# Optimization experiments

Measured on AMD Instinct MI355X. Metric: run time of the kernel, lower is better.

## Reference

```python
import jax, jax.numpy as jnp
import numpy as np

N = 8192
IN_DIM = 256
OUT_DIM = 128
ALPHA = 0.2  # LeakyReLU negative slope
MASK_VAL = -9e15


def setup_inputs() -> dict:
    key = jax.random.key(0)
    k1, k2, k3, k4 = jax.random.split(key, 4)
    adjacency = jax.random.randint(k1, (N, N), 0, 2, dtype=jnp.int32)
    X = jax.random.normal(k2, (N, IN_DIM), dtype=jnp.float32)
    # kaiming-normal-ish scale
    W = jax.random.normal(k3, (IN_DIM, OUT_DIM), dtype=jnp.float32) * np.sqrt(2.0 / IN_DIM)
    a = jax.random.normal(k4, (2 * OUT_DIM, 1), dtype=jnp.float32) * np.sqrt(2.0 / (2 * OUT_DIM))
    return {"adjacency": adjacency, "X": X, "W": W, "a": a}


def reference(adjacency, X, W, a):
    Wh = X @ W  # [N, D]
    # e[i,j] = lrelu([Wh_i ; Wh_j] @ a) = lrelu(Wh@a1 + (Wh@a2)^T)
    a1 = a[:OUT_DIM, 0]   # [D]
    a2 = a[OUT_DIM:, 0]   # [D]
    e = (Wh @ a1)[:, None] + (Wh @ a2)[None, :]  # [N, N]
    e = jax.nn.leaky_relu(e, negative_slope=ALPHA)
    scores = jnp.where(adjacency > 0, e, jnp.asarray(MASK_VAL, e.dtype))
    attention = jax.nn.softmax(scores, axis=1)  # dropout p=0 -> identity
    h_prime = attention @ Wh  # [N, D]
    return jax.nn.elu(h_prime)
```

## Files before the change

kernel.cpp:

```cpp
#include <hip/hip_runtime.h>
#include <hip/hip_bf16.h>

#define NN 8192
#define KDIM 256
#define DDIM 128

typedef __attribute__((ext_vector_type(8))) short short8;
typedef __attribute__((ext_vector_type(4))) float floatx4;
typedef __attribute__((ext_vector_type(4))) int intx4;

__device__ __forceinline__ unsigned short f2bf(float x) {
    unsigned int u = __float_as_uint(x);
    return (unsigned short)((u + 0x8000u) >> 16);
}

__global__ void k_trip(float* out, float v) {
    if (threadIdx.x == 0 && blockIdx.x == 0) out[0] = v;
}

__global__ void kA_swizzleW(const float* __restrict__ W, unsigned short* __restrict__ WB) {
    int gid = blockIdx.x * blockDim.x + threadIdx.x;
    int kt = gid >> 9, nt = (gid >> 6) & 7, lane = gid & 63;
    int quad = lane >> 4, c = lane & 15;
    short8 pack;
#pragma unroll
    for (int t = 0; t < 8; ++t)
        pack[t] = (short)f2bf(W[(kt * 32 + quad * 8 + t) * DDIM + nt * 16 + c]);
    *(short8*)(WB + ((size_t)(kt * 8 + nt) * 64 + lane) * 8) = pack;
}

__global__ __launch_bounds__(256) void kB_wh(
        const float* __restrict__ X,
        const unsigned short* __restrict__ WB,
        const float* __restrict__ a,
        unsigned short* __restrict__ WhB,
        float* __restrict__ f, float* __restrict__ g) {
    __shared__ unsigned short tile[64 * 128];
    int tid = threadIdx.x;
    int wave = tid >> 6, lane = tid & 63;
    int quad = lane >> 4, c = lane & 15;
    int rowbase = blockIdx.x * 64 + wave * 16;

    floatx4 acc[8];
#pragma unroll
    for (int nt = 0; nt < 8; ++nt) acc[nt] = (floatx4)(0.0f);

    const short8* WB8 = (const short8*)WB;
#pragma unroll
    for (int ks = 0; ks < 8; ++ks) {
        const float* xp = X + (size_t)(rowbase + c) * KDIM + ks * 32 + quad * 8;
        floatx4 x0 = *(const floatx4*)xp;
        floatx4 x1 = *(const floatx4*)(xp + 4);
        short8 afrag;
#pragma unroll
        for (int t = 0; t < 4; ++t) { afrag[t] = (short)f2bf(x0[t]); afrag[4 + t] = (short)f2bf(x1[t]); }
#pragma unroll
        for (int nt = 0; nt < 8; ++nt) {
            short8 b = WB8[(ks * 8 + nt) * 64 + lane];
            acc[nt] = __builtin_amdgcn_mfma_f32_16x16x32_bf16(afrag, b, acc[nt], 0, 0, 0);
        }
    }

    float fp[4] = {0.f, 0.f, 0.f, 0.f}, gp[4] = {0.f, 0.f, 0.f, 0.f};
#pragma unroll
    for (int nt = 0; nt < 8; ++nt) {
        float a1 = a[nt * 16 + c];
        float a2 = a[DDIM + nt * 16 + c];
#pragma unroll
        for (int r = 0; r < 4; ++r) {
            fp[r] += acc[nt][r] * a1;
            gp[r] += acc[nt][r] * a2;
        }
    }
#pragma unroll
    for (int m = 1; m < 16; m <<= 1) {
#pragma unroll
        for (int r = 0; r < 4; ++r) {
            fp[r] += __shfl_xor(fp[r], m);
            gp[r] += __shfl_xor(gp[r], m);
        }
    }
    if (c == 0) {
#pragma unroll
        for (int r = 0; r < 4; ++r) {
            f[rowbase + quad * 4 + r] = fp[r];
            g[rowbase + quad * 4 + r] = gp[r];
        }
    }

#pragma unroll
    for (int nt = 0; nt < 8; ++nt)
#pragma unroll
        for (int r = 0; r < 4; ++r)
            tile[(wave * 16 + quad * 4 + r) * 128 + nt * 16 + c] = f2bf(acc[nt][r]);
    __syncthreads();

    int kt2 = wave >> 1;
#pragma unroll
    for (int ntj = 0; ntj < 4; ++ntj) {
        int nt = (wave & 1) * 4 + ntj;
        short8 pack;
#pragma unroll
        for (int t = 0; t < 8; ++t)
            pack[t] = (short)tile[(kt2 * 32 + quad * 8 + t) * 128 + nt * 16 + c];
        *(short8*)(WhB + ((size_t)((blockIdx.x * 2 + kt2) * 8 + nt) * 64 + lane) * 8) = pack;
    }
}

__global__ __launch_bounds__(256, 4) void kC_attn2(
        const int* __restrict__ adj,
        const unsigned short* __restrict__ WhB,
        const float* __restrict__ f, const float* __restrict__ g,
        float* __restrict__ pacc, float* __restrict__ pl) {
    __shared__ float smem[8192];
    int tid = threadIdx.x;
    int wave = tid >> 6, lane = tid & 63;
    int quad = lane >> 4, c = lane & 15;
    int bq   = blockIdx.x >> 9;
    int brow = blockIdx.x & 511;
    int rowbase = brow * 16;

    {
        const floatx4* g4 = (const floatx4*)g;
        for (int i = tid; i < 1024; i += 256)
            ((floatx4*)smem)[i] = g4[bq * 1024 + i];
    }
    __syncthreads();

    float f0 = f[rowbase + c];

    floatx4 acc[8];
#pragma unroll
    for (int nt = 0; nt < 8; ++nt) acc[nt] = (floatx4)(0.0f);
    float l0 = 0.0f;

    const intx4* arow = (const intx4*)(adj + (size_t)(rowbase + c) * NN);
    const short8* WhB8 = (const short8*)WhB;
    int jbase = bq * 128;

    intx4 A0a = __builtin_nontemporal_load(&arow[(jbase + 0 * 4 + wave) * 8 + quad * 2]);
    intx4 A0b = __builtin_nontemporal_load(&arow[(jbase + 0 * 4 + wave) * 8 + quad * 2 + 1]);
    intx4 A1a = __builtin_nontemporal_load(&arow[(jbase + 1 * 4 + wave) * 8 + quad * 2]);
    intx4 A1b = __builtin_nontemporal_load(&arow[(jbase + 1 * 4 + wave) * 8 + quad * 2 + 1]);

    short8 bfrA[8], bfrB[8];
#pragma unroll
    for (int nt = 0; nt < 8; ++nt)
        bfrA[nt] = WhB8[((size_t)(jbase + wave) * 8 + nt) * 64 + lane];

#define KC_STEP(ITC, BCUR, BNEXT) do {                                          \
        int J32n_ = jbase + (((ITC) + 1) & 31) * 4 + wave;                      \
        _Pragma("unroll")                                                       \
        for (int nt = 0; nt < 8; ++nt)                                          \
            BNEXT[nt] = WhB8[((size_t)J32n_ * 8 + nt) * 64 + lane];             \
        int j4n_ = jbase + (((ITC) + 2) & 31) * 4 + wave;                       \
        intx4 A2a_ = __builtin_nontemporal_load(&arow[j4n_ * 8 + quad * 2]);    \
        intx4 A2b_ = __builtin_nontemporal_load(&arow[j4n_ * 8 + quad * 2 + 1]);\
        int gb_ = ((ITC) * 4 + wave) * 32 + quad * 8;                           \
        floatx4 g0_ = *(const floatx4*)&smem[gb_];                              \
        floatx4 g1_ = *(const floatx4*)&smem[gb_ + 4];                          \
        short8 afr_;                                                            \
        _Pragma("unroll")                                                       \
        for (int u = 0; u < 4; ++u) {                                           \
            float x_, E_;                                                       \
            x_ = f0 + g0_[u]; x_ = fmaxf(x_, 0.2f * x_);                        \
            E_ = (A0a[u] > 0) ? __expf(x_) : 0.0f; l0 += E_;                    \
            afr_[u] = (short)f2bf(E_);                                          \
            x_ = f0 + g1_[u]; x_ = fmaxf(x_, 0.2f * x_);                        \
            E_ = (A0b[u] > 0) ? __expf(x_) : 0.0f; l0 += E_;                    \
            afr_[4 + u] = (short)f2bf(E_);                                      \
        }                                                                       \
        _Pragma("unroll")                                                       \
        for (int nt = 0; nt < 8; ++nt)                                          \
            acc[nt] = __builtin_amdgcn_mfma_f32_16x16x32_bf16(afr_, BCUR[nt],   \
                                                              acc[nt], 0, 0, 0);\
        A0a = A1a; A0b = A1b; A1a = A2a_; A1b = A2b_;                           \
    } while (0)

    for (int it = 0; it < 32; it += 2) {
        KC_STEP(it, bfrA, bfrB);
        KC_STEP(it + 1, bfrB, bfrA);
    }
#undef KC_STEP

    __syncthreads();
    smem[7000 + wave * 64 + lane] = l0;
    __syncthreads();
    if (tid < 16) {
        float s = 0.0f;
#pragma unroll
        for (int w = 0; w < 4; ++w)
#pragma unroll
            for (int q = 0; q < 4; ++q)
                s += smem[7000 + w * 64 + q * 16 + tid];
        pl[bq * NN + rowbase + tid] = s;
    }

    if (wave >= 2) {
        float* b = &smem[(wave - 2) * 2304 + lane * 36];
#pragma unroll
        for (int nt = 0; nt < 8; ++nt) *(floatx4*)&b[nt * 4] = acc[nt];
    }
    __syncthreads();
    if (wave < 2) {
        float* b = &smem[wave * 2304 + lane * 36];
#pragma unroll
        for (int nt = 0; nt < 8; ++nt) acc[nt] += *(const floatx4*)&b[nt * 4];
    }
    __syncthreads();
    if (wave == 1) {
        float* b = &smem[lane * 36];
#pragma unroll
        for (int nt = 0; nt < 8; ++nt) *(floatx4*)&b[nt * 4] = acc[nt];
    }
    __syncthreads();

    if (wave == 0) {
        float* b = &smem[lane * 36];
#pragma unroll
        for (int nt = 0; nt < 8; ++nt) acc[nt] += *(const floatx4*)&b[nt * 4];
        float* pb = pacc + (size_t)bq * NN * DDIM;
#pragma unroll
        for (int nt = 0; nt < 8; ++nt)
#pragma unroll
            for (int r = 0; r < 4; ++r)
                pb[(size_t)(rowbase + quad * 4 + r) * DDIM + nt * 16 + c] = acc[nt][r];
    }
}

__global__ __launch_bounds__(256) void kD_merge2(
        const float* __restrict__ pacc, const float* __restrict__ pl,
        float* __restrict__ out) {
    int i = blockIdx.x * 256 + threadIdx.x;
    const floatx4* p4 = (const floatx4*)pacc;
    floatx4 a = p4[i];
    floatx4 b = p4[i + NN * DDIM / 4];
    int row = i >> 5;
    float s = pl[row] + pl[NN + row];
    float inv = (s > 0.0f) ? 1.0f / s : 0.0f;
    floatx4 h;
#pragma unroll
    for (int r = 0; r < 4; ++r) {
        float v = (a[r] + b[r]) * inv;
        h[r] = (v > 0.0f) ? v : expm1f(v);
    }
    ((floatx4*)out)[i] = h;
}

extern "C" void kernel_launch(void* const* d_in, const int* in_sizes, int n_in,
                              void* d_out, int out_size, void* d_ws, size_t ws_size,
                              hipStream_t stream) {
    float* out = (float*)d_out;

    const void *p_adj = nullptr, *p_X = nullptr, *p_W = nullptr, *p_a = nullptr;
    for (int i = 0; i < n_in; ++i) {
        switch (in_sizes[i]) {
            case NN * NN:     p_adj = d_in[i]; break;
            case NN * KDIM:   p_X   = d_in[i]; break;
            case KDIM * DDIM: p_W   = d_in[i]; break;
            case 2 * DDIM:    p_a   = d_in[i]; break;
            default: break;
        }
    }
    if (!p_adj || !p_X || !p_W || !p_a) {
        k_trip<<<dim3(1), dim3(64), 0, stream>>>(out, 99999.0f);
        return;
    }

    size_t off_WB   = 0;
    size_t off_WhB  = off_WB + 65536;
    size_t off_f    = off_WhB + (size_t)NN * DDIM * 2;
    size_t off_g    = off_f + NN * 4;
    size_t off_pacc = off_g + NN * 4;
    size_t off_pl   = off_pacc + (size_t)2 * NN * DDIM * 4;
    size_t needed   = off_pl + (size_t)2 * NN * 4;
    if (ws_size < needed) {
        k_trip<<<dim3(1), dim3(64), 0, stream>>>(out, 12345.0f);
        return;
    }
    char* ws = (char*)d_ws;
    unsigned short* WB   = (unsigned short*)(ws + off_WB);
    unsigned short* WhB  = (unsigned short*)(ws + off_WhB);
    float*          f    = (float*)(ws + off_f);
    float*          g    = (float*)(ws + off_g);
    float*          pacc = (float*)(ws + off_pacc);
    float*          pl   = (float*)(ws + off_pl);

    const int*   adj = (const int*)p_adj;
    const float* X   = (const float*)p_X;
    const float* W   = (const float*)p_W;
    const float* a   = (const float*)p_a;

    kA_swizzleW<<<dim3(16), dim3(256), 0, stream>>>(W, WB);
    kB_wh<<<dim3(128), dim3(256), 0, stream>>>(X, WB, a, WhB, f, g);
    kC_attn2<<<dim3(1024), dim3(256), 0, stream>>>(adj, WhB, f, g, pacc, pl);
    kD_merge2<<<dim3(NN * DDIM / 4 / 256), dim3(256), 0, stream>>>(pacc, pl, out);
}
```

Baseline: 435.7 us.

## Switch attention kernel to 32x32 MFMA with per-wave D split and 4-way column split

The attention kernel now uses 32x32x16 bf16 MFMA tiles covering 32 rows per block. Each wave owns a 32-column slice of the output dimension instead of a slice of the j range, so the cross-wave LDS reduction is removed. The j dimension is split four ways across blocks, and the merge kernel now sums four partials. The Wh swizzle layout is changed to match the 32x32 fragment format. The cost is that every wave recomputes the same exponentials for its rows, so exp work is duplicated four times, the adjacency loads lose their nontemporal hint, and partial-buffer traffic doubles.

```diff
diff --git a/kernel.cpp b/kernel.cpp
--- a/kernel.cpp
+++ b/kernel.cpp
@@ -7,6 +7,7 @@
 
 typedef __attribute__((ext_vector_type(8))) short short8;
 typedef __attribute__((ext_vector_type(4))) float floatx4;
+typedef __attribute__((ext_vector_type(16))) float floatx16;
 typedef __attribute__((ext_vector_type(4))) int intx4;
 
 __device__ __forceinline__ unsigned short f2bf(float x) {
@@ -95,153 +96,125 @@
             tile[(wave * 16 + quad * 4 + r) * 128 + nt * 16 + c] = f2bf(acc[nt][r]);
     __syncthreads();
 
-    int kt2 = wave >> 1;
-#pragma unroll
-    for (int ntj = 0; ntj < 4; ++ntj) {
-        int nt = (wave & 1) * 4 + ntj;
+    int half = lane >> 5, c32 = lane & 31;
+#pragma unroll
+    for (int dt = 0; dt < 4; ++dt) {
         short8 pack;
 #pragma unroll
         for (int t = 0; t < 8; ++t)
-            pack[t] = (short)tile[(kt2 * 32 + quad * 8 + t) * 128 + nt * 16 + c];
-        *(short8*)(WhB + ((size_t)((blockIdx.x * 2 + kt2) * 8 + nt) * 64 + lane) * 8) = pack;
-    }
-}
-
-__global__ __launch_bounds__(256, 4) void kC_attn2(
+            pack[t] = (short)tile[(wave * 16 + half * 8 + t) * 128 + dt * 32 + c32];
+        *(short8*)(WhB + ((size_t)((blockIdx.x * 4 + wave) * 4 + dt) * 64 + lane) * 8) = pack;
+    }
+}
+
+__global__ __launch_bounds__(256, 4) void kC_attn32(
         const int* __restrict__ adj,
         const unsigned short* __restrict__ WhB,
         const float* __restrict__ f, const float* __restrict__ g,
         float* __restrict__ pacc, float* __restrict__ pl) {
-    __shared__ float smem[8192];
+    __shared__ float smem[2048];
     int tid = threadIdx.x;
     int wave = tid >> 6, lane = tid & 63;
-    int quad = lane >> 4, c = lane & 15;
-    int bq   = blockIdx.x >> 9;
-    int brow = blockIdx.x & 511;
-    int rowbase = brow * 16;
+    int half = lane >> 5, r32 = lane & 31;
+    int bq   = blockIdx.x >> 8;
+    int brow = blockIdx.x & 255;
+    int rowbase = brow * 32;
 
     {
         const floatx4* g4 = (const floatx4*)g;
-        for (int i = tid; i < 1024; i += 256)
-            ((floatx4*)smem)[i] = g4[bq * 1024 + i];
+        for (int i = tid; i < 512; i += 256)
+            ((floatx4*)smem)[i] = g4[bq * 512 + i];
     }
     __syncthreads();
 
-    float f0 = f[rowbase + c];
-
-    floatx4 acc[8];
-#pragma unroll
-    for (int nt = 0; nt < 8; ++nt) acc[nt] = (floatx4)(0.0f);
+    float f0 = f[rowbase + r32];
+
+    floatx16 acc = (floatx16)(0.0f);
     float l0 = 0.0f;
 
-    const intx4* arow = (const intx4*)(adj + (size_t)(rowbase + c) * NN);
+    const intx4* arow = (const intx4*)(adj + (size_t)(rowbase + r32) * NN);
     const short8* WhB8 = (const short8*)WhB;
-    int jbase = bq * 128;
-
-    intx4 A0a = __builtin_nontemporal_load(&arow[(jbase + 0 * 4 + wave) * 8 + quad * 2]);
-    intx4 A0b = __builtin_nontemporal_load(&arow[(jbase + 0 * 4 + wave) * 8 + quad * 2 + 1]);
-    intx4 A1a = __builtin_nontemporal_load(&arow[(jbase + 1 * 4 + wave) * 8 + quad * 2]);
-    intx4 A1b = __builtin_nontemporal_load(&arow[(jbase + 1 * 4 + wave) * 8 + quad * 2 + 1]);
-
-    short8 bfrA[8], bfrB[8];
-#pragma unroll
-    for (int nt = 0; nt < 8; ++nt)
-        bfrA[nt] = WhB8[((size_t)(jbase + wave) * 8 + nt) * 64 + lane];
-
-#define KC_STEP(ITC, BCUR, BNEXT) do {                                          \
-        int J32n_ = jbase + (((ITC) + 1) & 31) * 4 + wave;                      \
-        _Pragma("unroll")                                                       \
-        for (int nt = 0; nt < 8; ++nt)                                          \
-            BNEXT[nt] = WhB8[((size_t)J32n_ * 8 + nt) * 64 + lane];             \
-        int j4n_ = jbase + (((ITC) + 2) & 31) * 4 + wave;                       \
-        intx4 A2a_ = __builtin_nontemporal_load(&arow[j4n_ * 8 + quad * 2]);    \
-        intx4 A2b_ = __builtin_nontemporal_load(&arow[j4n_ * 8 + quad * 2 + 1]);\
-        int gb_ = ((ITC) * 4 + wave) * 32 + quad * 8;                           \
+    int jb = bq * 64;
+
+    intx4 A00, A01, A02, A03, A10, A11, A12, A13;
+    {
+        int i0 = (jb + 0) * 8 + half * 2;
+        A00 = arow[i0]; A01 = arow[i0 + 1]; A02 = arow[i0 + 4]; A03 = arow[i0 + 5];
+        int i1 = (jb + 1) * 8 + half * 2;
+        A10 = arow[i1]; A11 = arow[i1 + 1]; A12 = arow[i1 + 4]; A13 = arow[i1 + 5];
+    }
+
+    short8 bfrA0, bfrA1, bfrB0, bfrB1;
+    bfrA0 = WhB8[((size_t)((jb + 0) * 2 + 0) * 4 + wave) * 64 + lane];
+    bfrA1 = WhB8[((size_t)((jb + 0) * 2 + 1) * 4 + wave) * 64 + lane];
+
+#define KC_STEP(ITC, BC0, BC1, BN0, BN1) do {                                   \
+        int J32n_ = jb + (((ITC) + 1) & 63);                                    \
+        BN0 = WhB8[((size_t)(J32n_ * 2 + 0) * 4 + wave) * 64 + lane];           \
+        BN1 = WhB8[((size_t)(J32n_ * 2 + 1) * 4 + wave) * 64 + lane];           \
+        int ja_ = (jb + (((ITC) + 2) & 63)) * 8 + half * 2;                     \
+        intx4 L0_ = arow[ja_],     L1_ = arow[ja_ + 1];                         \
+        intx4 L2_ = arow[ja_ + 4], L3_ = arow[ja_ + 5];                         \
+        int gb_ = (ITC) * 32 + half * 8;                                        \
         floatx4 g0_ = *(const floatx4*)&smem[gb_];                              \
         floatx4 g1_ = *(const floatx4*)&smem[gb_ + 4];                          \
-        short8 afr_;                                                            \
+        floatx4 g2_ = *(const floatx4*)&smem[gb_ + 16];                         \
+        floatx4 g3_ = *(const floatx4*)&smem[gb_ + 20];                         \
+        short8 af0_, af1_;                                                      \
         _Pragma("unroll")                                                       \
         for (int u = 0; u < 4; ++u) {                                           \
             float x_, E_;                                                       \
             x_ = f0 + g0_[u]; x_ = fmaxf(x_, 0.2f * x_);                        \
-            E_ = (A0a[u] > 0) ? __expf(x_) : 0.0f; l0 += E_;                    \
-            afr_[u] = (short)f2bf(E_);                                          \
+            E_ = (A00[u] > 0) ? __expf(x_) : 0.0f; l0 += E_;                    \
+            af0_[u] = (short)f2bf(E_);                                          \
             x_ = f0 + g1_[u]; x_ = fmaxf(x_, 0.2f * x_);                        \
-            E_ = (A0b[u] > 0) ? __expf(x_) : 0.0f; l0 += E_;                    \
-            afr_[4 + u] = (short)f2bf(E_);                                      \
+            E_ = (A01[u] > 0) ? __expf(x_) : 0.0f; l0 += E_;                    \
+            af0_[4 + u] = (short)f2bf(E_);                                      \
+            x_ = f0 + g2_[u]; x_ = fmaxf(x_, 0.2f * x_);                        \
+            E_ = (A02[u] > 0) ? __expf(x_) : 0.0f; l0 += E_;                    \
+            af1_[u] = (short)f2bf(E_);                                          \
+            x_ = f0 + g3_[u]; x_ = fmaxf(x_, 0.2f * x_);                        \
+            E_ = (A03[u] > 0) ? __expf(x_) : 0.0f; l0 += E_;                    \
+            af1_[4 + u] = (short)f2bf(E_);                                      \
         }                                                                       \
-        _Pragma("unroll")                                                       \
-        for (int nt = 0; nt < 8; ++nt)                                          \
-            acc[nt] = __builtin_amdgcn_mfma_f32_16x16x32_bf16(afr_, BCUR[nt],   \
-                                                              acc[nt], 0, 0, 0);\
-        A0a = A1a; A0b = A1b; A1a = A2a_; A1b = A2b_;                           \
+        acc = __builtin_amdgcn_mfma_f32_32x32x16_bf16(af0_, BC0, acc, 0, 0, 0); \
+        acc = __builtin_amdgcn_mfma_f32_32x32x16_bf16(af1_, BC1, acc, 0, 0, 0); \
+        A00 = A10; A01 = A11; A02 = A12; A03 = A13;                             \
+        A10 = L0_; A11 = L1_; A12 = L2_; A13 = L3_;                             \
     } while (0)
 
-    for (int it = 0; it < 32; it += 2) {
-        KC_STEP(it, bfrA, bfrB);
-        KC_STEP(it + 1, bfrB, bfrA);
+    for (int it = 0; it < 64; it += 2) {
+        KC_STEP(it, bfrA0, bfrA1, bfrB0, bfrB1);
+        KC_STEP(it + 1, bfrB0, bfrB1, bfrA0, bfrA1);
     }
 #undef KC_STEP
 
-    __syncthreads();
-    smem[7000 + wave * 64 + lane] = l0;
-    __syncthreads();
-    if (tid < 16) {
-        float s = 0.0f;
-#pragma unroll
-        for (int w = 0; w < 4; ++w)
-#pragma unroll
-            for (int q = 0; q < 4; ++q)
-                s += smem[7000 + w * 64 + q * 16 + tid];
-        pl[bq * NN + rowbase + tid] = s;
-    }
-
-    if (wave >= 2) {
-        float* b = &smem[(wave - 2) * 2304 + lane * 36];
-#pragma unroll
-        for (int nt = 0; nt < 8; ++nt) *(floatx4*)&b[nt * 4] = acc[nt];
-    }
-    __syncthreads();
-    if (wave < 2) {
-        float* b = &smem[wave * 2304 + lane * 36];
-#pragma unroll
-        for (int nt = 0; nt < 8; ++nt) acc[nt] += *(const floatx4*)&b[nt * 4];
-    }
-    __syncthreads();
-    if (wave == 1) {
-        float* b = &smem[lane * 36];
-#pragma unroll
-        for (int nt = 0; nt < 8; ++nt) *(floatx4*)&b[nt * 4] = acc[nt];
-    }
-    __syncthreads();
-
-    if (wave == 0) {
-        float* b = &smem[lane * 36];
-#pragma unroll
-        for (int nt = 0; nt < 8; ++nt) acc[nt] += *(const floatx4*)&b[nt * 4];
-        float* pb = pacc + (size_t)bq * NN * DDIM;
-#pragma unroll
-        for (int nt = 0; nt < 8; ++nt)
-#pragma unroll
-            for (int r = 0; r < 4; ++r)
-                pb[(size_t)(rowbase + quad * 4 + r) * DDIM + nt * 16 + c] = acc[nt][r];
-    }
-}
-
-__global__ __launch_bounds__(256) void kD_merge2(
+    float lsum = l0 + __shfl_xor(l0, 32);
+    if (wave == 0 && lane < 32)
+        pl[bq * NN + rowbase + lane] = lsum;
+
+    float* pb = pacc + (size_t)bq * NN * DDIM;
+#pragma unroll
+    for (int reg = 0; reg < 16; ++reg) {
+        int irow = (reg & 3) + 8 * (reg >> 2) + 4 * half;
+        pb[(size_t)(rowbase + irow) * DDIM + wave * 32 + r32] = acc[reg];
+    }
+}
+
+__global__ __launch_bounds__(256) void kD_merge4(
         const float* __restrict__ pacc, const float* __restrict__ pl,
         float* __restrict__ out) {
     int i = blockIdx.x * 256 + threadIdx.x;
+    const int Q = NN * DDIM / 4;
     const floatx4* p4 = (const floatx4*)pacc;
-    floatx4 a = p4[i];
-    floatx4 b = p4[i + NN * DDIM / 4];
+    floatx4 a0 = p4[i], a1 = p4[i + Q], a2 = p4[i + 2 * Q], a3 = p4[i + 3 * Q];
     int row = i >> 5;
-    float s = pl[row] + pl[NN + row];
+    float s = pl[row] + pl[NN + row] + pl[2 * NN + row] + pl[3 * NN + row];
     float inv = (s > 0.0f) ? 1.0f / s : 0.0f;
     floatx4 h;
 #pragma unroll
     for (int r = 0; r < 4; ++r) {
-        float v = (a[r] + b[r]) * inv;
+        float v = (a0[r] + a1[r] + a2[r] + a3[r]) * inv;
         h[r] = (v > 0.0f) ? v : expm1f(v);
     }
     ((floatx4*)out)[i] = h;
@@ -272,8 +245,8 @@
     size_t off_f    = off_WhB + (size_t)NN * DDIM * 2;
     size_t off_g    = off_f + NN * 4;
     size_t off_pacc = off_g + NN * 4;
-    size_t off_pl   = off_pacc + (size_t)2 * NN * DDIM * 4;
-    size_t needed   = off_pl + (size_t)2 * NN * 4;
+    size_t off_pl   = off_pacc + (size_t)4 * NN * DDIM * 4;
+    size_t needed   = off_pl + (size_t)4 * NN * 4;
     if (ws_size < needed) {
         k_trip<<<dim3(1), dim3(64), 0, stream>>>(out, 12345.0f);
         return;
@@ -293,6 +266,6 @@
 
     kA_swizzleW<<<dim3(16), dim3(256), 0, stream>>>(W, WB);
     kB_wh<<<dim3(128), dim3(256), 0, stream>>>(X, WB, a, WhB, f, g);
-    kC_attn2<<<dim3(1024), dim3(256), 0, stream>>>(adj, WhB, f, g, pacc, pl);
-    kD_merge2<<<dim3(NN * DDIM / 4 / 256), dim3(256), 0, stream>>>(pacc, pl, out);
-}
+    kC_attn32<<<dim3(1024), dim3(256), 0, stream>>>(adj, WhB, f, g, pacc, pl);
+    kD_merge4<<<dim3(NN * DDIM / 4 / 256), dim3(256), 0, stream>>>(pacc, pl, out);
+}
```

Result: slower. 453.2 us (+4.0%).
